# Optimization experiments

Measured on AMD Instinct MI355X. Metric: run time of the kernel, lower is better.

Reference implementation:

```python
import jax, jax.numpy as jnp
import numpy as np

LORA_ALPHA = 16.0
TOP_K = 2


def setup_inputs() -> dict:
    key = jax.random.key(0)
    k_x, k_w, k_g, k_a, k_b = jax.random.split(key, 5)
    B, S, H, O, E, R = 2, 2048, 2048, 2048, 8, 16
    x = jax.random.normal(k_x, (B, S, H), dtype=jnp.float32)
    weight = jax.random.normal(k_w, (O, H), dtype=jnp.float32)          # frozen base W [out, in]
    gate_w = jax.random.normal(k_g, (E, H), dtype=jnp.float32) * 0.02   # router gate [E, in]
    A_w = jax.random.normal(k_a, (E, R, H), dtype=jnp.float32) * (1.0 / np.sqrt(H))  # stacked lora_A
    B_w = jax.random.normal(k_b, (E, O, R), dtype=jnp.float32) * 0.01   # stacked lora_B
    return {"x": x, "weight": weight, "gate_w": gate_w, "A_w": A_w, "B_w": B_w}


def reference(x, weight, gate_w, A_w, B_w):
    E = gate_w.shape[0]
    # Base frozen linear: F.linear(x, weight)
    out = jnp.einsum("bsh,oh->bso", x, weight)

    # Router: softmax over experts, top-2, renormalize
    logits = jnp.einsum("bsh,eh->bse", x, gate_w)
    probs = jax.nn.softmax(logits, axis=-1)
    topk_w, topk_idx = jax.lax.top_k(probs, TOP_K)          # [b,s,2]
    topk_w = topk_w / jnp.sum(topk_w, axis=-1, keepdims=True)

    # Per-token combine weight for each expert (sum over the 2 slots)
    onehot = jax.nn.one_hot(topk_idx, E, dtype=x.dtype)      # [b,s,2,E]
    cw = jnp.einsum("bsk,bske->bse", topk_w, onehot)         # [b,s,E]

    # LoRA: down-project into all experts' rank spaces, weight, then up-project.
    # t: [b,s,E,r] is small (r=16); weighting here avoids a [b,s,E,out] buffer.
    t = jnp.einsum("bsh,erh->bser", x, A_w)
    t = t * cw[..., None]
    lora = jnp.einsum("bser,eor->bso", t, B_w)

    return out + LORA_ALPHA * lora
```

## Files before the change

### kernel.cpp

```cpp
#include <hip/hip_runtime.h>
#include <hip/hip_bf16.h>


typedef __bf16 bf16x8 __attribute__((ext_vector_type(8)));
typedef float f32x4 __attribute__((ext_vector_type(4)));

__device__ __forceinline__ __bf16 f2bf(float f) {
  union { float f; unsigned u; } v; v.f = f;
  unsigned r = (v.u + 0x7FFFu + ((v.u >> 16) & 1u)) >> 16;
  unsigned short s = (unsigned short)r;
  return __builtin_bit_cast(__bf16, s);
}

__device__ __forceinline__ void ld_lds16(const void* g, void* l) {
  __builtin_amdgcn_global_load_lds((__attribute__((address_space(1))) void*)g,
                                   (__attribute__((address_space(3))) void*)l,
                                   16, 0, 0);
}

__global__ void prep_kernel(const float* __restrict__ W, const float* __restrict__ Aw,
                            const float* __restrict__ Bw, __bf16* __restrict__ Bfull,
                            __bf16* __restrict__ A2) {
  const int b = blockIdx.x, tid = threadIdx.x;
  if (b < 2176) {
    const float* src = (b < 2048) ? (W + (size_t)b * 2048)
                                  : (Aw + (size_t)(b - 2048) * 2048);
    __bf16* dst = (b < 2048) ? (Bfull + (size_t)b * 2176)
                             : (A2 + (size_t)(b - 2048) * 2048);
    const int c = tid * 8;
    float4 a = *(const float4*)(src + c);
    float4 d = *(const float4*)(src + c + 4);
    bf16x8 v;
    v[0] = f2bf(a.x); v[1] = f2bf(a.y); v[2] = f2bf(a.z); v[3] = f2bf(a.w);
    v[4] = f2bf(d.x); v[5] = f2bf(d.y); v[6] = f2bf(d.z); v[7] = f2bf(d.w);
    *(bf16x8*)(dst + c) = v;
  } else {
    const int idx = (b - 2176) * 256 + tid;
    const int e = idx >> 11, o = idx & 2047;
    const float4* s = (const float4*)(Bw + ((size_t)e * 2048 + o) * 16);
    float4 v0 = s[0], v1 = s[1], v2 = s[2], v3 = s[3];
    __bf16* d = Bfull + (size_t)o * 2176 + 2048 + e * 16;
    bf16x8 lo, hi;
    lo[0] = f2bf(v0.x); lo[1] = f2bf(v0.y); lo[2] = f2bf(v0.z); lo[3] = f2bf(v0.w);
    lo[4] = f2bf(v1.x); lo[5] = f2bf(v1.y); lo[6] = f2bf(v1.z); lo[7] = f2bf(v1.w);
    hi[0] = f2bf(v2.x); hi[1] = f2bf(v2.y); hi[2] = f2bf(v2.z); hi[3] = f2bf(v2.w);
    hi[4] = f2bf(v3.x); hi[5] = f2bf(v3.y); hi[6] = f2bf(v3.z); hi[7] = f2bf(v3.w);
    *(bf16x8*)d = lo;
    *(bf16x8*)(d + 8) = hi;
  }
}

__global__ __launch_bounds__(256) void router_t2(
    const float* __restrict__ x, const float* __restrict__ gw,
    const __bf16* __restrict__ A2, __bf16* __restrict__ Abuf) {
  __shared__ __align__(16) __bf16 xs[16][2056];
  __shared__ float red[4][16][8];
  __shared__ float cws[16][8];
  const int tid = threadIdx.x;
  const int wave = tid >> 6, lane = tid & 63;
  const int t0 = blockIdx.x * 16;

#pragma unroll 4
  for (int i = 0; i < 16; ++i) {
    const float* xr = x + (size_t)(t0 + i) * 2048 + tid * 8;
    float4 a = *(const float4*)xr;
    float4 b = *(const float4*)(xr + 4);
    bf16x8 v;
    v[0] = f2bf(a.x); v[1] = f2bf(a.y); v[2] = f2bf(a.z); v[3] = f2bf(a.w);
    v[4] = f2bf(b.x); v[5] = f2bf(b.y); v[6] = f2bf(b.z); v[7] = f2bf(b.w);
    *(bf16x8*)(Abuf + (size_t)(t0 + i) * 2176 + tid * 8) = v;
    *(bf16x8*)&xs[i][tid * 8] = v;
  }
  __syncthreads();

  const int tok = tid & 15, slc = tid >> 4;
  const int c0 = slc * 128;
  float acc[8] = {0, 0, 0, 0, 0, 0, 0, 0};
  for (int j8 = 0; j8 < 16; ++j8) {
    bf16x8 xv = *(const bf16x8*)&xs[tok][c0 + j8 * 8];
    float xf[8];
#pragma unroll
    for (int j = 0; j < 8; ++j) xf[j] = (float)xv[j];
#pragma unroll
    for (int e = 0; e < 8; ++e) {
      float4 g0 = *(const float4*)(gw + e * 2048 + c0 + j8 * 8);
      float4 g1 = *(const float4*)(gw + e * 2048 + c0 + j8 * 8 + 4);
      acc[e] += xf[0] * g0.x + xf[1] * g0.y + xf[2] * g0.z + xf[3] * g0.w +
                xf[4] * g1.x + xf[5] * g1.y + xf[6] * g1.z + xf[7] * g1.w;
    }
  }
#pragma unroll
  for (int e = 0; e < 8; ++e) {
    acc[e] += __shfl_down(acc[e], 16);
    acc[e] += __shfl_down(acc[e], 32);
  }
  if (lane < 16) {
#pragma unroll
    for (int e = 0; e < 8; ++e) red[wave][lane][e] = acc[e];
  }
  __syncthreads();
  if (tid < 16) {
    float lg[8];
#pragma unroll
    for (int e = 0; e < 8; ++e)
      lg[e] = red[0][tid][e] + red[1][tid][e] + red[2][tid][e] + red[3][tid][e];
    int a = 0;
    for (int e = 1; e < 8; ++e) if (lg[e] > lg[a]) a = e;
    int b = (a == 0) ? 1 : 0;
    for (int e = 0; e < 8; ++e) if (e != a && lg[e] > lg[b]) b = e;
    const float d = __expf(lg[b] - lg[a]);
    float o[8] = {0, 0, 0, 0, 0, 0, 0, 0};
    o[a] = 1.0f / (1.0f + d);
    o[b] = d / (1.0f + d);
#pragma unroll
    for (int e = 0; e < 8; ++e) cws[tid][e] = o[e];
  }
  __syncthreads();

  const int m = lane & 15, q = lane >> 4;
  const int nt0 = wave * 2;
  f32x4 tacc[2] = {};
  for (int ks = 0; ks < 64; ++ks) {
    bf16x8 af = *(const bf16x8*)&xs[m][ks * 32 + q * 8];
#pragma unroll
    for (int h = 0; h < 2; ++h) {
      bf16x8 bfg = *(const bf16x8*)(A2 + (size_t)((nt0 + h) * 16 + m) * 2048 +
                                    ks * 32 + q * 8);
      tacc[h] = __builtin_amdgcn_mfma_f32_16x16x32_bf16(af, bfg, tacc[h], 0, 0, 0);
    }
  }
#pragma unroll
  for (int h = 0; h < 2; ++h) {
    const int nt = nt0 + h;
#pragma unroll
    for (int rg = 0; rg < 4; ++rg) {
      const int trow = q * 4 + rg;
      const float s = tacc[h][rg] * 16.0f * cws[trow][nt];
      Abuf[(size_t)(t0 + trow) * 2176 + 2048 + nt * 16 + m] = f2bf(s);
    }
  }
}

__global__ __launch_bounds__(128, 2) void mfma_gemm_bt(
    const __bf16* __restrict__ A, const __bf16* __restrict__ B,
    float* __restrict__ C, int lda, int ldb, int ldc, int kiters) {
  __shared__ __align__(16) __bf16 As[128 * 64];
  __shared__ __align__(16) __bf16 Bs[64 * 64];
  const int tid = threadIdx.x;
  const int wave = tid >> 6;
  const int lane = tid & 63;
  const int tm = blockIdx.x * 128;
  const int tn = blockIdx.y * 64;

  const int wm = wave * 64;
  const int srow = lane >> 3;
  const int skoff = ((lane & 7) ^ srow) * 8;

  const int rlo = lane & 7;
  const int rb3 = (lane >> 3) & 1;
  const int qb = lane >> 4;

  f32x4 acc[4][4] = {};

  int kcur = 0;
  for (int kt = 0; kt < kiters; ++kt) {
#pragma unroll
    for (int r = 0; r < 8; ++r) {
      const int ch = r * 2 + wave;
      ld_lds16(A + (size_t)(tm + ch * 8 + srow) * lda + kcur + skoff, &As[ch * 512]);
    }
#pragma unroll
    for (int r = 0; r < 4; ++r) {
      const int ch = r * 2 + wave;
      ld_lds16(B + (size_t)(tn + ch * 8 + srow) * ldb + kcur + skoff, &Bs[ch * 512]);
    }
    __syncthreads();
#pragma unroll
    for (int ks = 0; ks < 2; ++ks) {
      bf16x8 af[4], bfg[4];
      const int q8 = ((ks * 4 + qb) ^ rlo) * 8;
#pragma unroll
      for (int i = 0; i < 4; ++i) {
        const int rh = ((wm + i * 16) >> 3) + rb3;
        af[i] = *(const bf16x8*)&As[rh * 512 + rlo * 64 + q8];
      }
#pragma unroll
      for (int j = 0; j < 4; ++j) {
        const int rh = ((j * 16) >> 3) + rb3;
        bfg[j] = *(const bf16x8*)&Bs[rh * 512 + rlo * 64 + q8];
      }
#pragma unroll
      for (int i = 0; i < 4; ++i)
#pragma unroll
        for (int j = 0; j < 4; ++j)
          acc[i][j] = __builtin_amdgcn_mfma_f32_16x16x32_bf16(af[i], bfg[j], acc[i][j], 0, 0, 0);
    }
    __syncthreads();
    kcur += 64;
  }

  const int crow0 = tm + wm + (lane >> 4) * 4;
  const int ccol0 = tn + (lane & 15);
#pragma unroll
  for (int i = 0; i < 4; ++i)
#pragma unroll
    for (int j = 0; j < 4; ++j)
#pragma unroll
      for (int rg = 0; rg < 4; ++rg)
        C[(size_t)(crow0 + i * 16 + rg) * ldc + ccol0 + j * 16] = acc[i][j][rg];
}

extern "C" void kernel_launch(void* const* d_in, const int* in_sizes, int n_in,
                              void* d_out, int out_size, void* d_ws, size_t ws_size,
                              hipStream_t stream) {
  const float* x = (const float*)d_in[0];
  const float* weight = (const float*)d_in[1];
  const float* gate_w = (const float*)d_in[2];
  const float* A_w = (const float*)d_in[3];
  const float* B_w = (const float*)d_in[4];
  float* out = (float*)d_out;

  char* ws = (char*)d_ws;
  __bf16* Abuf = (__bf16*)ws;
  __bf16* Bfull = (__bf16*)(ws + 17825792);
  __bf16* A2 = (__bf16*)(ws + 26738688);

  prep_kernel<<<2240, 256, 0, stream>>>(weight, A_w, B_w, Bfull, A2);
  router_t2<<<256, 256, 0, stream>>>(x, gate_w, A2, Abuf);
  mfma_gemm_bt<<<dim3(32, 32), 128, 0, stream>>>(Abuf, Bfull, out, 2176, 2176,
                                                 2048, 34);
}
```

Before: 168.5 us.

## Rewrite main GEMM with 256x128 tiles, triple-buffered LDS prefetch, and block swizzle

```diff
diff --git a/kernel.cpp b/kernel.cpp
--- a/kernel.cpp
+++ b/kernel.cpp
@@ -141,66 +141,92 @@
   }
 }
 
-__global__ __launch_bounds__(128, 2) void mfma_gemm_bt(
+__global__ __launch_bounds__(512, 2) void mfma_gemm_bt2(
     const __bf16* __restrict__ A, const __bf16* __restrict__ B,
     float* __restrict__ C, int lda, int ldb, int ldc, int kiters) {
-  __shared__ __align__(16) __bf16 As[128 * 64];
-  __shared__ __align__(16) __bf16 Bs[64 * 64];
+  __shared__ __align__(16) __bf16 lds[3 * 24576];
   const int tid = threadIdx.x;
   const int wave = tid >> 6;
   const int lane = tid & 63;
-  const int tm = blockIdx.x * 128;
-  const int tn = blockIdx.y * 64;
-
-  const int wm = wave * 64;
+
+  const int wg = blockIdx.x + (blockIdx.y << 4);
+  const int swz = (wg & 7) * 32 + (wg >> 3);
+  const int tm = (swz & 15) * 256;
+  const int tn = (swz >> 4) * 128;
+
   const int srow = lane >> 3;
   const int skoff = ((lane & 7) ^ srow) * 8;
 
+  const int wr = wave >> 1, wc = wave & 1;
   const int rlo = lane & 7;
   const int rb3 = (lane >> 3) & 1;
   const int qb = lane >> 4;
 
   f32x4 acc[4][4] = {};
 
-  int kcur = 0;
+  auto stage = [&](int buf, int kt) {
+    const int kc = kt * 64;
+    __bf16* Ls = lds + buf * 24576;
+#pragma unroll
+    for (int r = 0; r < 4; ++r) {
+      const int ch = wave + r * 8;
+      ld_lds16(A + (size_t)(tm + ch * 8 + srow) * lda + kc + skoff, &Ls[ch * 512]);
+    }
+#pragma unroll
+    for (int r = 0; r < 2; ++r) {
+      const int ch = wave + r * 8;
+      ld_lds16(B + (size_t)(tn + ch * 8 + srow) * ldb + kc + skoff,
+               &Ls[16384 + ch * 512]);
+    }
+  };
+
+  stage(0, 0);
+  stage(1, 1);
+  asm volatile("s_waitcnt vmcnt(6)" ::: "memory");
+  __builtin_amdgcn_s_barrier();
+
+  int cb = 0;
   for (int kt = 0; kt < kiters; ++kt) {
-#pragma unroll
-    for (int r = 0; r < 8; ++r) {
-      const int ch = r * 2 + wave;
-      ld_lds16(A + (size_t)(tm + ch * 8 + srow) * lda + kcur + skoff, &As[ch * 512]);
-    }
-#pragma unroll
-    for (int r = 0; r < 4; ++r) {
-      const int ch = r * 2 + wave;
-      ld_lds16(B + (size_t)(tn + ch * 8 + srow) * ldb + kcur + skoff, &Bs[ch * 512]);
-    }
-    __syncthreads();
+    const bool pf = (kt + 2 < kiters);
+    if (pf) stage((kt + 2) % 3, kt + 2);
+
+    const __bf16* As = lds + cb * 24576;
+    const __bf16* Bs = As + 16384;
 #pragma unroll
     for (int ks = 0; ks < 2; ++ks) {
       bf16x8 af[4], bfg[4];
       const int q8 = ((ks * 4 + qb) ^ rlo) * 8;
 #pragma unroll
       for (int i = 0; i < 4; ++i) {
-        const int rh = ((wm + i * 16) >> 3) + rb3;
+        const int rh = wr * 8 + i * 2 + rb3;
         af[i] = *(const bf16x8*)&As[rh * 512 + rlo * 64 + q8];
       }
 #pragma unroll
       for (int j = 0; j < 4; ++j) {
-        const int rh = ((j * 16) >> 3) + rb3;
+        const int rh = wc * 8 + j * 2 + rb3;
         bfg[j] = *(const bf16x8*)&Bs[rh * 512 + rlo * 64 + q8];
       }
+      __builtin_amdgcn_s_setprio(1);
 #pragma unroll
       for (int i = 0; i < 4; ++i)
 #pragma unroll
         for (int j = 0; j < 4; ++j)
-          acc[i][j] = __builtin_amdgcn_mfma_f32_16x16x32_bf16(af[i], bfg[j], acc[i][j], 0, 0, 0);
-    }
-    __syncthreads();
-    kcur += 64;
-  }
-
-  const int crow0 = tm + wm + (lane >> 4) * 4;
-  const int ccol0 = tn + (lane & 15);
+          acc[i][j] =
+              __builtin_amdgcn_mfma_f32_16x16x32_bf16(af[i], bfg[j], acc[i][j], 0, 0, 0);
+      __builtin_amdgcn_s_setprio(0);
+    }
+    asm volatile("s_waitcnt lgkmcnt(0)" ::: "memory");
+    if (pf) {
+      asm volatile("s_waitcnt vmcnt(6)" ::: "memory");
+    } else {
+      asm volatile("s_waitcnt vmcnt(0)" ::: "memory");
+    }
+    __builtin_amdgcn_s_barrier();
+    cb = (cb + 1 == 3) ? 0 : cb + 1;
+  }
+
+  const int crow0 = tm + wr * 64 + (lane >> 4) * 4;
+  const int ccol0 = tn + wc * 64 + (lane & 15);
 #pragma unroll
   for (int i = 0; i < 4; ++i)
 #pragma unroll
@@ -227,6 +253,6 @@
 
   prep_kernel<<<2240, 256, 0, stream>>>(weight, A_w, B_w, Bfull, A2);
   router_t2<<<256, 256, 0, stream>>>(x, gate_w, A2, Abuf);
-  mfma_gemm_bt<<<dim3(32, 32), 128, 0, stream>>>(Abuf, Bfull, out, 2176, 2176,
-                                                 2048, 34);
-}
+  mfma_gemm_bt2<<<dim3(16, 16), 512, 0, stream>>>(Abuf, Bfull, out, 2176, 2176,
+                                                  2048, 34);
+}
```

New measurement: 164.7 us. 2.3% less time.
